# Kernel optimization log

Measured on AMD Instinct MI355X. Metric: run time of the kernel, lower is better.

Reference implementation:

```python
import jax, jax.numpy as jnp
import numpy as np

N_NODES = 100000
N_EDGES = 1600000
D_IN = 256
D_OUT = 128


def setup_inputs() -> dict:
    key = jax.random.key(0)
    k1, k2, k3, k4, k5, k6 = jax.random.split(key, 6)
    inp = {
        "input": jax.random.normal(k1, (N_NODES, D_IN), dtype=jnp.float32),
        "edge_row": jax.random.randint(k2, (N_EDGES,), 0, N_NODES),
        "edge_col": jax.random.randint(k3, (N_EDGES,), 0, N_NODES),
        "edge_val": jax.random.uniform(k4, (N_EDGES,), dtype=jnp.float32),
        "W": jax.random.normal(k5, (D_IN, D_OUT), dtype=jnp.float32) * (1.0 / np.sqrt(D_IN)),
        "b": jax.random.normal(k6, (D_OUT,), dtype=jnp.float32) * 0.01,
    }
    return inp


def reference(input, edge_row, edge_col, edge_val, W, b):
    # support = Linear(input)  -> [N, D_OUT]
    support = jnp.dot(input, W) + b
    # sparse.mm(adj, support): out[r] = sum_e val[e] * support[col[e]] for edges with row[e]==r
    msgs = edge_val[:, None] * support[edge_col]  # [E, D_OUT]
    agg = jax.ops.segment_sum(msgs, edge_row, num_segments=N_NODES)  # [N, D_OUT]
    return jnp.tanh(agg)
```

## Files before the change

kernel.cpp:

```cpp
#include <hip/hip_runtime.h>
#include <math.h>

#define N_NODES 100000
#define N_EDGES 1600000
#define D_IN 256
#define D_OUT 128

#define OFF_SUPPORT 0
#define OFF_COUNTS  51200000
#define OFF_CSREV   51600008
#define OFF_BSUMS   64400008

#define SCAN_CHUNK  1024
#define SCAN_BLOCKS ((N_NODES + SCAN_CHUNK - 1) / SCAN_CHUNK)

#define GB 128
#define GEMM_BLOCKS ((N_NODES + GB - 1) / GB)
#define GEMM_SPLIT  391
#define EDGE_BLOCKS ((N_EDGES + 255) / 256)

#define AP 40

typedef __attribute__((ext_vector_type(8))) short s8v;
typedef __attribute__((ext_vector_type(4))) float f4v;

__device__ __forceinline__ short f2bf(float x) {
  unsigned u = __float_as_uint(x);
  unsigned r = u + 0x7FFF + ((u >> 16) & 1);
  return (short)(r >> 16);
}
__device__ __forceinline__ float bf2f(short h) {
  return __uint_as_float(((unsigned)(unsigned short)h) << 16);
}

__device__ __forceinline__ void gemm_body(
    int gb, const float* __restrict__ input, const float* __restrict__ W,
    const float* __restrict__ b, float* __restrict__ support) {
  __shared__ short Ahi[GB * AP];
  __shared__ short Alo[GB * AP];
  __shared__ short Bhi[D_OUT * AP];
  __shared__ short Blo[D_OUT * AP];

  const int t = threadIdx.x;
  const int node0 = gb * GB;
  const int lane = t & 63;
  const int wv = t >> 6;
  const int qm = lane & 15;
  const int quad = lane >> 4;

  f4v acc[2][8];
#pragma unroll
  for (int mt = 0; mt < 2; mt++)
#pragma unroll
    for (int nt = 0; nt < 8; nt++) acc[mt][nt] = (f4v){0.f, 0.f, 0.f, 0.f};

  for (int k0 = 0; k0 < D_IN; k0 += 32) {
#pragma unroll
    for (int j = 0; j < 4; j++) {
      int i = t + j * 256;
      int row = i >> 3;
      int kf = (i & 7) << 2;
      int node = node0 + row;
      float4 v = make_float4(0.f, 0.f, 0.f, 0.f);
      if (node < N_NODES)
        v = *(const float4*)(input + (size_t)node * D_IN + k0 + kf);
      short4 h, l;
      h.x = f2bf(v.x); l.x = f2bf(v.x - bf2f(h.x));
      h.y = f2bf(v.y); l.y = f2bf(v.y - bf2f(h.y));
      h.z = f2bf(v.z); l.z = f2bf(v.z - bf2f(h.z));
      h.w = f2bf(v.w); l.w = f2bf(v.w - bf2f(h.w));
      *(short4*)&Ahi[row * AP + kf] = h;
      *(short4*)&Alo[row * AP + kf] = l;
    }
#pragma unroll
    for (int j = 0; j < 4; j++) {
      int i = t + j * 256;
      int kk = i >> 5;
      int nf = (i & 31) << 2;
      float4 v = *(const float4*)(W + (size_t)(k0 + kk) * D_OUT + nf);
      float vv[4] = {v.x, v.y, v.z, v.w};
#pragma unroll
      for (int c = 0; c < 4; c++) {
        short h = f2bf(vv[c]);
        Bhi[(nf + c) * AP + kk] = h;
        Blo[(nf + c) * AP + kk] = f2bf(vv[c] - bf2f(h));
      }
    }
    __syncthreads();

    s8v ah0 = *(s8v*)&Ahi[(wv * 32 + qm) * AP + quad * 8];
    s8v al0 = *(s8v*)&Alo[(wv * 32 + qm) * AP + quad * 8];
    s8v ah1 = *(s8v*)&Ahi[(wv * 32 + 16 + qm) * AP + quad * 8];
    s8v al1 = *(s8v*)&Alo[(wv * 32 + 16 + qm) * AP + quad * 8];
#pragma unroll
    for (int nt = 0; nt < 8; nt++) {
      s8v bh = *(s8v*)&Bhi[(nt * 16 + qm) * AP + quad * 8];
      s8v bl = *(s8v*)&Blo[(nt * 16 + qm) * AP + quad * 8];
      acc[0][nt] = __builtin_amdgcn_mfma_f32_16x16x32_bf16(ah0, bh, acc[0][nt], 0, 0, 0);
      acc[0][nt] = __builtin_amdgcn_mfma_f32_16x16x32_bf16(ah0, bl, acc[0][nt], 0, 0, 0);
      acc[0][nt] = __builtin_amdgcn_mfma_f32_16x16x32_bf16(al0, bh, acc[0][nt], 0, 0, 0);
      acc[1][nt] = __builtin_amdgcn_mfma_f32_16x16x32_bf16(ah1, bh, acc[1][nt], 0, 0, 0);
      acc[1][nt] = __builtin_amdgcn_mfma_f32_16x16x32_bf16(ah1, bl, acc[1][nt], 0, 0, 0);
      acc[1][nt] = __builtin_amdgcn_mfma_f32_16x16x32_bf16(al1, bh, acc[1][nt], 0, 0, 0);
    }
    __syncthreads();
  }

  float bias[8];
#pragma unroll
  for (int nt = 0; nt < 8; nt++) bias[nt] = b[nt * 16 + qm];
#pragma unroll
  for (int mt = 0; mt < 2; mt++) {
#pragma unroll
    for (int nt = 0; nt < 8; nt++) {
      int col = nt * 16 + qm;
#pragma unroll
      for (int r = 0; r < 4; r++) {
        int node = node0 + wv * 32 + mt * 16 + quad * 4 + r;
        if (node < N_NODES)
          support[(size_t)node * D_OUT + col] = acc[mt][nt][r] + bias[nt];
      }
    }
  }
}

__global__ __launch_bounds__(256) void gemm_hist_kernel(
    const float* __restrict__ input, const float* __restrict__ W,
    const float* __restrict__ b, float* __restrict__ support,
    const int* __restrict__ erow, int* __restrict__ counts,
    int* __restrict__ pos_e) {
  if (blockIdx.x < GEMM_SPLIT) {
    gemm_body(blockIdx.x, input, W, b, support);
  } else {
    int e = (blockIdx.x - GEMM_SPLIT) * 256 + threadIdx.x;
    if (e < N_EDGES) pos_e[e] = atomicAdd(&counts[erow[e]], 1);
  }
}

__global__ __launch_bounds__(256) void gemm_build_kernel(
    const float* __restrict__ input, const float* __restrict__ W,
    const float* __restrict__ b, float* __restrict__ support,
    const int* __restrict__ erow, const int* __restrict__ ecol,
    const float* __restrict__ eval, const int* __restrict__ offsets,
    const int* __restrict__ pos_e, int2* __restrict__ csr_ev) {
  if (blockIdx.x < GEMM_BLOCKS - GEMM_SPLIT) {
    gemm_body(blockIdx.x + GEMM_SPLIT, input, W, b, support);
  } else {
    int e = (blockIdx.x - (GEMM_BLOCKS - GEMM_SPLIT)) * 256 + threadIdx.x;
    if (e < N_EDGES) {
      int idx = offsets[erow[e]] + pos_e[e];
      csr_ev[idx] = make_int2(ecol[e], __float_as_int(eval[e]));
    }
  }
}

__global__ __launch_bounds__(256) void scan_phase1(const int* __restrict__ counts,
                                                   int* __restrict__ bsums) {
  __shared__ int ts[256];
  int t = threadIdx.x;
  int idx0 = blockIdx.x * SCAN_CHUNK + t * 4;
  int s = 0;
#pragma unroll
  for (int i = 0; i < 4; i++)
    if (idx0 + i < N_NODES) s += counts[idx0 + i];
  ts[t] = s;
  __syncthreads();
#pragma unroll
  for (int off = 128; off > 0; off >>= 1) {
    if (t < off) ts[t] += ts[t + off];
    __syncthreads();
  }
  if (t == 0) bsums[blockIdx.x] = ts[0];
}

__global__ __launch_bounds__(128) void scan_phase2(int* __restrict__ bsums) {
  __shared__ int s[128];
  int t = threadIdx.x;
  int v = (t < SCAN_BLOCKS) ? bsums[t] : 0;
  s[t] = v;
  __syncthreads();
#pragma unroll
  for (int off = 1; off < 128; off <<= 1) {
    int x = (t >= off) ? s[t - off] : 0;
    __syncthreads();
    s[t] += x;
    __syncthreads();
  }
  if (t < SCAN_BLOCKS) bsums[t] = s[t] - v;
}

__global__ __launch_bounds__(256) void scan_phase3(int* __restrict__ counts,
                                                   const int* __restrict__ bsums) {
  __shared__ int ts[256];
  int t = threadIdx.x;
  int b = blockIdx.x;
  int idx0 = b * SCAN_CHUNK + t * 4;
  int v[4];
  int s = 0;
#pragma unroll
  for (int i = 0; i < 4; i++) {
    v[i] = (idx0 + i < N_NODES) ? counts[idx0 + i] : 0;
    s += v[i];
  }
  ts[t] = s;
  __syncthreads();
#pragma unroll
  for (int off = 1; off < 256; off <<= 1) {
    int x = (t >= off) ? ts[t - off] : 0;
    __syncthreads();
    ts[t] += x;
    __syncthreads();
  }
  int run = bsums[b] + ts[t] - s;
#pragma unroll
  for (int i = 0; i < 4; i++) {
    int idx = idx0 + i;
    if (idx < N_NODES) counts[idx] = run;
    run += v[i];
  }
  if (b == 0 && t == 0) counts[N_NODES] = N_EDGES;
}

__global__ __launch_bounds__(128) void agg_kernel(
    const int* __restrict__ offsets, const int2* __restrict__ csr_ev,
    const float* __restrict__ support, float* __restrict__ out) {
  int r = blockIdx.x;
  int f = threadIdx.x;
  int beg = offsets[r];
  int end = offsets[r + 1];
  float acc = 0.f;
  int j = beg;
  for (; j + 4 <= end; j += 4) {
    int2 e0 = csr_ev[j + 0];
    int2 e1 = csr_ev[j + 1];
    int2 e2 = csr_ev[j + 2];
    int2 e3 = csr_ev[j + 3];
    float s0 = support[(size_t)e0.x * D_OUT + f];
    float s1 = support[(size_t)e1.x * D_OUT + f];
    float s2 = support[(size_t)e2.x * D_OUT + f];
    float s3 = support[(size_t)e3.x * D_OUT + f];
    acc = fmaf(__int_as_float(e0.y), s0, acc);
    acc = fmaf(__int_as_float(e1.y), s1, acc);
    acc = fmaf(__int_as_float(e2.y), s2, acc);
    acc = fmaf(__int_as_float(e3.y), s3, acc);
  }
  for (; j < end; j++) {
    int2 ev = csr_ev[j];
    acc = fmaf(__int_as_float(ev.y), support[(size_t)ev.x * D_OUT + f], acc);
  }
  out[(size_t)r * D_OUT + f] = tanhf(acc);
}

extern "C" void kernel_launch(void* const* d_in, const int* in_sizes, int n_in,
                              void* d_out, int out_size, void* d_ws, size_t ws_size,
                              hipStream_t stream) {
  const float* input = (const float*)d_in[0];
  const int* erow = (const int*)d_in[1];
  const int* ecol = (const int*)d_in[2];
  const float* eval = (const float*)d_in[3];
  const float* W = (const float*)d_in[4];
  const float* b = (const float*)d_in[5];
  float* out = (float*)d_out;

  char* ws = (char*)d_ws;
  float* support = (float*)(ws + OFF_SUPPORT);
  int* counts = (int*)(ws + OFF_COUNTS);
  int2* csr_ev = (int2*)(ws + OFF_CSREV);
  int* bsums = (int*)(ws + OFF_BSUMS);
  int* pos_e = (int*)d_out;

  hipMemsetAsync(ws + OFF_COUNTS, 0, (size_t)(N_NODES + 1) * 4, stream);

  hipLaunchKernelGGL(gemm_hist_kernel, dim3(GEMM_SPLIT + EDGE_BLOCKS), dim3(256),
                     0, stream, input, W, b, support, erow, counts, pos_e);
  hipLaunchKernelGGL(scan_phase1, dim3(SCAN_BLOCKS), dim3(256), 0, stream,
                     counts, bsums);
  hipLaunchKernelGGL(scan_phase2, dim3(1), dim3(128), 0, stream, bsums);
  hipLaunchKernelGGL(scan_phase3, dim3(SCAN_BLOCKS), dim3(256), 0, stream,
                     counts, bsums);
  hipLaunchKernelGGL(gemm_build_kernel,
                     dim3((GEMM_BLOCKS - GEMM_SPLIT) + EDGE_BLOCKS), dim3(256),
                     0, stream, input, W, b, support, erow, ecol, eval, counts,
                     pos_e, csr_ev);
  hipLaunchKernelGGL(agg_kernel, dim3(N_NODES), dim3(128), 0, stream, counts,
                     csr_ev, support, out);
}
```

Measured before the change: 433.0 us.

## Pre-convert W to split-bf16 once, move all GEMM into hist kernel, unroll agg by 8

A small kernel now converts W once into transposed bf16 hi/lo arrays, so each GEMM block loads B tiles with vector copies instead of redoing float-to-bf16 conversion and scattered LDS stores. All GEMM blocks now run alongside the histogram atomics, and the CSR build kernel is edge-only. The aggregation loop is unrolled to 8 gathers in flight. The cost is one extra launch, and the schedule change removes the overlap of GEMM with the CSR build step.

Measured after the change: 420.7 us. 1.03x faster.

```diff
diff --git a/kernel.cpp b/kernel.cpp
--- a/kernel.cpp
+++ b/kernel.cpp
@@ -10,13 +10,14 @@
 #define OFF_COUNTS  51200000
 #define OFF_CSREV   51600008
 #define OFF_BSUMS   64400008
+#define OFF_WTHI    64400416
+#define OFF_WTLO    64465952
 
 #define SCAN_CHUNK  1024
 #define SCAN_BLOCKS ((N_NODES + SCAN_CHUNK - 1) / SCAN_CHUNK)
 
 #define GB 128
 #define GEMM_BLOCKS ((N_NODES + GB - 1) / GB)
-#define GEMM_SPLIT  391
 #define EDGE_BLOCKS ((N_EDGES + 255) / 256)
 
 #define AP 40
@@ -33,9 +34,22 @@
   return __uint_as_float(((unsigned)(unsigned short)h) << 16);
 }
 
+__global__ __launch_bounds__(256) void wconv_kernel(
+    const float* __restrict__ W, short* __restrict__ wt_hi,
+    short* __restrict__ wt_lo) {
+  int idx = blockIdx.x * 256 + threadIdx.x;
+  int k = idx >> 7;
+  int n = idx & 127;
+  float v = W[idx];
+  short h = f2bf(v);
+  wt_hi[n * 256 + k] = h;
+  wt_lo[n * 256 + k] = f2bf(v - bf2f(h));
+}
+
 __device__ __forceinline__ void gemm_body(
-    int gb, const float* __restrict__ input, const float* __restrict__ W,
-    const float* __restrict__ b, float* __restrict__ support) {
+    int gb, const float* __restrict__ input, const short* __restrict__ wt_hi,
+    const short* __restrict__ wt_lo, const float* __restrict__ b,
+    float* __restrict__ support) {
   __shared__ short Ahi[GB * AP];
   __shared__ short Alo[GB * AP];
   __shared__ short Bhi[D_OUT * AP];
@@ -73,18 +87,12 @@
       *(short4*)&Alo[row * AP + kf] = l;
     }
 #pragma unroll
-    for (int j = 0; j < 4; j++) {
+    for (int j = 0; j < 2; j++) {
       int i = t + j * 256;
-      int kk = i >> 5;
-      int nf = (i & 31) << 2;
-      float4 v = *(const float4*)(W + (size_t)(k0 + kk) * D_OUT + nf);
-      float vv[4] = {v.x, v.y, v.z, v.w};
-#pragma unroll
-      for (int c = 0; c < 4; c++) {
-        short h = f2bf(vv[c]);
-        Bhi[(nf + c) * AP + kk] = h;
-        Blo[(nf + c) * AP + kk] = f2bf(vv[c] - bf2f(h));
-      }
+      int n = i >> 2;
+      int kq = (i & 3) << 3;
+      *(s8v*)&Bhi[n * AP + kq] = *(const s8v*)&wt_hi[n * 256 + k0 + kq];
+      *(s8v*)&Blo[n * AP + kq] = *(const s8v*)&wt_lo[n * 256 + k0 + kq];
     }
     __syncthreads();
 
@@ -125,32 +133,26 @@
 }
 
 __global__ __launch_bounds__(256) void gemm_hist_kernel(
-    const float* __restrict__ input, const float* __restrict__ W,
-    const float* __restrict__ b, float* __restrict__ support,
-    const int* __restrict__ erow, int* __restrict__ counts,
-    int* __restrict__ pos_e) {
-  if (blockIdx.x < GEMM_SPLIT) {
-    gemm_body(blockIdx.x, input, W, b, support);
+    const float* __restrict__ input, const short* __restrict__ wt_hi,
+    const short* __restrict__ wt_lo, const float* __restrict__ b,
+    float* __restrict__ support, const int* __restrict__ erow,
+    int* __restrict__ counts, int* __restrict__ pos_e) {
+  if (blockIdx.x < GEMM_BLOCKS) {
+    gemm_body(blockIdx.x, input, wt_hi, wt_lo, b, support);
   } else {
-    int e = (blockIdx.x - GEMM_SPLIT) * 256 + threadIdx.x;
+    int e = (blockIdx.x - GEMM_BLOCKS) * 256 + threadIdx.x;
     if (e < N_EDGES) pos_e[e] = atomicAdd(&counts[erow[e]], 1);
   }
 }
 
-__global__ __launch_bounds__(256) void gemm_build_kernel(
-    const float* __restrict__ input, const float* __restrict__ W,
-    const float* __restrict__ b, float* __restrict__ support,
+__global__ __launch_bounds__(256) void build_kernel(
     const int* __restrict__ erow, const int* __restrict__ ecol,
     const float* __restrict__ eval, const int* __restrict__ offsets,
     const int* __restrict__ pos_e, int2* __restrict__ csr_ev) {
-  if (blockIdx.x < GEMM_BLOCKS - GEMM_SPLIT) {
-    gemm_body(blockIdx.x + GEMM_SPLIT, input, W, b, support);
-  } else {
-    int e = (blockIdx.x - (GEMM_BLOCKS - GEMM_SPLIT)) * 256 + threadIdx.x;
-    if (e < N_EDGES) {
-      int idx = offsets[erow[e]] + pos_e[e];
-      csr_ev[idx] = make_int2(ecol[e], __float_as_int(eval[e]));
-    }
+  int e = blockIdx.x * 256 + threadIdx.x;
+  if (e < N_EDGES) {
+    int idx = offsets[erow[e]] + pos_e[e];
+    csr_ev[idx] = make_int2(ecol[e], __float_as_int(eval[e]));
   }
 }
 
@@ -230,19 +232,15 @@
   int end = offsets[r + 1];
   float acc = 0.f;
   int j = beg;
-  for (; j + 4 <= end; j += 4) {
-    int2 e0 = csr_ev[j + 0];
-    int2 e1 = csr_ev[j + 1];
-    int2 e2 = csr_ev[j + 2];
-    int2 e3 = csr_ev[j + 3];
-    float s0 = support[(size_t)e0.x * D_OUT + f];
-    float s1 = support[(size_t)e1.x * D_OUT + f];
-    float s2 = support[(size_t)e2.x * D_OUT + f];
-    float s3 = support[(size_t)e3.x * D_OUT + f];
-    acc = fmaf(__int_as_float(e0.y), s0, acc);
-    acc = fmaf(__int_as_float(e1.y), s1, acc);
-    acc = fmaf(__int_as_float(e2.y), s2, acc);
-    acc = fmaf(__int_as_float(e3.y), s3, acc);
+  for (; j + 8 <= end; j += 8) {
+    int2 e[8];
+    float s[8];
+#pragma unroll
+    for (int u = 0; u < 8; u++) e[u] = csr_ev[j + u];
+#pragma unroll
+    for (int u = 0; u < 8; u++) s[u] = support[(size_t)e[u].x * D_OUT + f];
+#pragma unroll
+    for (int u = 0; u < 8; u++) acc = fmaf(__int_as_float(e[u].y), s[u], acc);
   }
   for (; j < end; j++) {
     int2 ev = csr_ev[j];
@@ -267,21 +265,24 @@
   int* counts = (int*)(ws + OFF_COUNTS);
   int2* csr_ev = (int2*)(ws + OFF_CSREV);
   int* bsums = (int*)(ws + OFF_BSUMS);
+  short* wt_hi = (short*)(ws + OFF_WTHI);
+  short* wt_lo = (short*)(ws + OFF_WTLO);
   int* pos_e = (int*)d_out;
 
+  hipLaunchKernelGGL(wconv_kernel, dim3((D_IN * D_OUT) / 256), dim3(256), 0,
+                     stream, W, wt_hi, wt_lo);
   hipMemsetAsync(ws + OFF_COUNTS, 0, (size_t)(N_NODES + 1) * 4, stream);
 
-  hipLaunchKernelGGL(gemm_hist_kernel, dim3(GEMM_SPLIT + EDGE_BLOCKS), dim3(256),
-                     0, stream, input, W, b, support, erow, counts, pos_e);
+  hipLaunchKernelGGL(gemm_hist_kernel, dim3(GEMM_BLOCKS + EDGE_BLOCKS),
+                     dim3(256), 0, stream, input, wt_hi, wt_lo, b, support,
+                     erow, counts, pos_e);
   hipLaunchKernelGGL(scan_phase1, dim3(SCAN_BLOCKS), dim3(256), 0, stream,
                      counts, bsums);
   hipLaunchKernelGGL(scan_phase2, dim3(1), dim3(128), 0, stream, bsums);
   hipLaunchKernelGGL(scan_phase3, dim3(SCAN_BLOCKS), dim3(256), 0, stream,
                      counts, bsums);
-  hipLaunchKernelGGL(gemm_build_kernel,
-                     dim3((GEMM_BLOCKS - GEMM_SPLIT) + EDGE_BLOCKS), dim3(256),
-                     0, stream, input, W, b, support, erow, ecol, eval, counts,
-                     pos_e, csr_ev);
+  hipLaunchKernelGGL(build_kernel, dim3(EDGE_BLOCKS), dim3(256), 0, stream,
+                     erow, ecol, eval, counts, pos_e, csr_ev);
   hipLaunchKernelGGL(agg_kernel, dim3(N_NODES), dim3(128), 0, stream, counts,
                      csr_ev, support, out);
 }
```
